# Optimization experiments

Hardware: AMD Instinct MI355X
Metric: run time of the kernel (lower is better)

## Reference

```python
import jax, jax.numpy as jnp
import numpy as np

EPS = 1e-6

def setup_inputs() -> dict:
    key = jax.random.key(0)
    ks = jax.random.split(key, 8)
    I, S, O = 1024, 512, 1024
    Bsz, T = 4, 2048
    return {
        "u": jax.random.normal(ks[0], (Bsz, T, I), dtype=jnp.float32),
        "dt": jax.random.normal(ks[1], (S,), dtype=jnp.float32),
        "A": jax.random.normal(ks[2], (S,), dtype=jnp.float32),
        "Bmat": jax.random.normal(ks[3], (I, S), dtype=jnp.float32) / np.sqrt(S),
        "C": jax.random.normal(ks[4], (S, O), dtype=jnp.float32) / np.sqrt(S),
        "D": jax.random.normal(ks[5], (O,), dtype=jnp.float32),
        "norm_w": jnp.ones((I,), dtype=jnp.float32),
    }

def _rmsnorm(x, w):
    x32 = x.astype(jnp.float32)
    n = x32 * jax.lax.rsqrt(jnp.mean(x32 * x32, axis=-1, keepdims=True) + EPS)
    return n.astype(x.dtype) * w

def reference(u, dt, A, Bmat, C, D, norm_w):
    u = _rmsnorm(u, norm_w)                      # [B, T, I]
    Bsz, T, _ = u.shape
    dts = jax.nn.sigmoid(dt)                     # [S]
    a = jnp.exp(-dts * jnp.abs(A))               # [S] discretized decay
    t = jnp.arange(T, dtype=jnp.float32)
    h = dts[:, None] * a[:, None] ** t[None, :]  # [S, T] geometric kernel
    u_proj = jnp.einsum('bti,is->bst', u, Bmat)  # [B, S, T]
    # depthwise causal conv: flipped kernel + cross-correlation == convolution
    k = jnp.flip(h, axis=1)[:, None, :]          # [S, 1, T] (OIW)
    x = jax.lax.conv_general_dilated(
        u_proj, k, window_strides=(1,), padding=[(T - 1, T - 1)],
        dimension_numbers=('NCW', 'OIW', 'NCW'),
        feature_group_count=u_proj.shape[1])[:, :, :T]  # [B, S, T]
    x = jnp.transpose(x, (0, 2, 1))              # [B, T, S]
    y = jnp.einsum('bts,so->bto', x, C) + D      # [B, T, O]
    return (y, x[:, -1])
```

## Files before the change

kernel.cpp:

```cpp
#include <hip/hip_runtime.h>
#include <math.h>

#define I_DIM 1024
#define S_DIM 512
#define O_DIM 1024
#define T_DIM 2048
#define B_SZ 4
#define M_ROWS (B_SZ * T_DIM)
#define EPSF 1e-6f

#define CL 64
#define NCH 32

typedef _Float16 f16;
typedef __attribute__((ext_vector_type(8))) _Float16 f16x8;
typedef __attribute__((ext_vector_type(2))) _Float16 f16x2;
typedef __attribute__((ext_vector_type(4))) float f32x4;

__device__ __forceinline__ unsigned short f2h_bits(float f) {
    _Float16 h = (_Float16)f;
    return __builtin_bit_cast(unsigned short, h);
}

__device__ __forceinline__ void load16_lds(const void* g, void* l) {
    __builtin_amdgcn_global_load_lds((const __attribute__((address_space(1))) void*)g,
                                     (__attribute__((address_space(3))) void*)l,
                                     16, 0, 0);
}

__global__ __launch_bounds__(256)
void prep(const float* __restrict__ u, const float* __restrict__ nw,
          unsigned short* __restrict__ u16,
          const float* __restrict__ Bmat, const float* __restrict__ dt,
          unsigned short* __restrict__ Bt16,
          const float* __restrict__ Cmat, unsigned short* __restrict__ Ct16) {
    __shared__ float tile[32][33];
    const int t = threadIdx.x;
    const int bx = blockIdx.x;

    if (bx < M_ROWS) {
        float4 v = ((const float4*)(u + (size_t)bx * I_DIM))[t];
        float ss = v.x * v.x + v.y * v.y + v.z * v.z + v.w * v.w;
        #pragma unroll
        for (int off = 32; off > 0; off >>= 1) ss += __shfl_down(ss, off, 64);
        if ((t & 63) == 0) tile[0][t >> 6] = ss;
        __syncthreads();
        if (t == 0)
            tile[0][0] = rsqrtf((tile[0][0] + tile[0][1] + tile[0][2] + tile[0][3])
                                * (1.0f / I_DIM) + EPSF);
        __syncthreads();
        const float rs = tile[0][0];
        float4 w = ((const float4*)nw)[t];
        ushort4 o;
        o.x = f2h_bits(v.x * rs * w.x);
        o.y = f2h_bits(v.y * rs * w.y);
        o.z = f2h_bits(v.z * rs * w.z);
        o.w = f2h_bits(v.w * rs * w.w);
        ((ushort4*)(u16 + (size_t)bx * I_DIM))[t] = o;
    } else if (bx < M_ROWS + 512) {
        const int tb = bx - M_ROWS;
        const int bs = (tb & 15) * 32;
        const int bi = (tb >> 4) * 32;
        const int tx = t & 31, ty = t >> 5;
        #pragma unroll
        for (int i = ty; i < 32; i += 8)
            tile[i][tx] = Bmat[(size_t)(bi + i) * S_DIM + bs + tx];
        __syncthreads();
        #pragma unroll
        for (int i = ty; i < 32; i += 8) {
            const int s = bs + i;
            const float dts = 1.0f / (1.0f + expf(-dt[s]));
            Bt16[(size_t)s * I_DIM + bi + tx] = f2h_bits(tile[tx][i] * dts);
        }
    } else {
        const int tb = bx - M_ROWS - 512;
        const int bo = (tb & 31) * 32;
        const int bs = (tb >> 5) * 32;
        const int tx = t & 31, ty = t >> 5;
        #pragma unroll
        for (int i = ty; i < 32; i += 8)
            tile[i][tx] = Cmat[(size_t)(bs + i) * O_DIM + bo + tx];
        __syncthreads();
        #pragma unroll
        for (int i = ty; i < 32; i += 8)
            Ct16[(size_t)(bo + i) * S_DIM + bs + tx] = f2h_bits(tile[tx][i]);
    }
}

template<bool BIAS, bool CHFIN, typename OUT>
__global__ __launch_bounds__(256)
void mfma_gemm_f16(const f16* __restrict__ A, const f16* __restrict__ Bt,
                   OUT* __restrict__ Cout, int M, int N, int K, int ldb,
                   const float* __restrict__ bias,
                   const float* __restrict__ dt, const float* __restrict__ Avec,
                   float* __restrict__ chlast) {
    constexpr int BM = 64, BN = 128;
    __shared__ f16 As[2][BM * 32];
    __shared__ f16 Bs[2][BN * 32];
    const int t = threadIdx.x;

    int bid = blockIdx.y * gridDim.x + blockIdx.x;
    const int nwg = gridDim.x * gridDim.y;
    const int cpx = nwg >> 3;
    bid = (bid & 7) * cpx + (bid >> 3);
    const int n0 = (bid % gridDim.x) * BN;
    const int m0 = (bid / gridDim.x) * BM;

    const int wid = t >> 6, lane = t & 63;
    const int wn = wid * 32;
    const int lr = lane & 15, kg = lane >> 4;

    f32x4 acc[4][2];
    #pragma unroll
    for (int i = 0; i < 4; ++i)
        #pragma unroll
        for (int j = 0; j < 2; ++j) acc[i][j] = (f32x4){0.f, 0.f, 0.f, 0.f};

    const size_t arow = (size_t)(m0 + (t >> 2)) * K + (t & 3) * 8;
    const size_t brow = (size_t)(n0 + (t >> 2)) * ldb + (t & 3) * 8;

    auto stage = [&](int k0, int bsel) {
        load16_lds(A + arow + k0, &As[bsel][t * 8]);
        load16_lds(Bt + brow + k0, &Bs[bsel][t * 8]);
        load16_lds(Bt + brow + (size_t)64 * ldb + k0, &Bs[bsel][2048 + t * 8]);
    };

    const int nk = K >> 5;
    stage(0, 0);
    for (int kt = 0; kt < nk; ++kt) {
        const int cur = kt & 1;
        if (kt + 1 < nk) {
            stage((kt + 1) << 5, cur ^ 1);
            asm volatile("s_waitcnt vmcnt(3)");
        } else {
            asm volatile("s_waitcnt vmcnt(0)");
        }
        __builtin_amdgcn_s_barrier();
        __builtin_amdgcn_sched_barrier(0);

        f16x8 af[4], bfr[2];
        #pragma unroll
        for (int m = 0; m < 4; ++m)
            af[m] = *(const f16x8*)&As[cur][(m * 16 + lr) * 32 + kg * 8];
        #pragma unroll
        for (int n = 0; n < 2; ++n)
            bfr[n] = *(const f16x8*)&Bs[cur][(wn + n * 16 + lr) * 32 + kg * 8];
        #pragma unroll
        for (int m = 0; m < 4; ++m)
            #pragma unroll
            for (int n = 0; n < 2; ++n)
                acc[m][n] = __builtin_amdgcn_mfma_f32_16x16x32_f16(af[m], bfr[n], acc[m][n], 0, 0, 0);
        __builtin_amdgcn_s_barrier();
    }

    #pragma unroll
    for (int m = 0; m < 4; ++m) {
        const int row = m0 + m * 16 + kg * 4;
        #pragma unroll
        for (int n = 0; n < 2; ++n) {
            const int col = n0 + wn + n * 16 + lr;
            const float b = BIAS ? bias[col] : 0.0f;
            #pragma unroll
            for (int j = 0; j < 4; ++j) {
                if constexpr (sizeof(OUT) == 4)
                    Cout[(size_t)(row + j) * N + col] = (OUT)(acc[m][n][j] + b);
                else
                    Cout[(size_t)(row + j) * N + col] = (OUT)(_Float16)acc[m][n][j];
            }
        }
    }

    if constexpr (CHFIN) {
        const int cb = m0 >> 11;
        const int cc = (m0 >> 6) & (NCH - 1);
        #pragma unroll
        for (int n = 0; n < 2; ++n) {
            const int s = n0 + wn + n * 16 + lr;
            const float dts = 1.0f / (1.0f + expf(-dt[s]));
            const float e = dts * fabsf(Avec[s]);
            const float ainv = expf(e);
            float partial = 0.f;
            #pragma unroll
            for (int m = 0; m < 4; ++m) {
                float wgt = expf(-e * (float)(63 - m * 16 - kg * 4));
                #pragma unroll
                for (int j = 0; j < 4; ++j) {
                    partial = fmaf(wgt, acc[m][n][j], partial);
                    wgt *= ainv;
                }
            }
            partial += __shfl_xor(partial, 16, 64);
            partial += __shfl_xor(partial, 32, 64);
            if (kg == 0)
                chlast[(size_t)(cb * NCH + cc) * S_DIM + s] = partial;
        }
    }
}

__global__ __launch_bounds__(256)
void scan_apply(const f16* __restrict__ up, const float* __restrict__ chlast,
                const float* __restrict__ dt, const float* __restrict__ Avec,
                unsigned* __restrict__ x32, float* __restrict__ xlast) {
    const int gid = blockIdx.x * 256 + threadIdx.x;
    const int s2 = gid & 255;
    const int c = (gid >> 8) & (NCH - 1);
    const int b = gid >> 13;
    const int s0 = s2 * 2;
    const float dts0 = 1.0f / (1.0f + expf(-dt[s0]));
    const float dts1 = 1.0f / (1.0f + expf(-dt[s0 + 1]));
    const float ab0 = fabsf(Avec[s0]), ab1 = fabsf(Avec[s0 + 1]);
    const float a0 = expf(-dts0 * ab0);
    const float a1 = expf(-dts1 * ab1);
    const float aCL0 = expf(-dts0 * ab0 * (float)CL);
    const float aCL1 = expf(-dts1 * ab1 * (float)CL);

    const float2* ch = (const float2*)chlast;
    float cy0 = 0.f, cy1 = 0.f;
    for (int j = 0; j < c; ++j) {
        float2 f = ch[(size_t)(b * NCH + j) * 256 + s2];
        cy0 = fmaf(aCL0, cy0, f.x);
        cy1 = fmaf(aCL1, cy1, f.y);
    }

    const unsigned* up32 = (const unsigned*)up;
    const size_t base = (size_t)(b * T_DIM + c * CL) * 256 + s2;
    unsigned v[CL];
    #pragma unroll
    for (int j = 0; j < CL; ++j) v[j] = up32[base + (size_t)j * 256];
    float x0 = cy0, x1 = cy1;
    #pragma unroll
    for (int j = 0; j < CL; ++j) {
        f16x2 h = __builtin_bit_cast(f16x2, v[j]);
        x0 = fmaf(a0, x0, (float)h.x);
        x1 = fmaf(a1, x1, (float)h.y);
        f16x2 o; o.x = (_Float16)x0; o.y = (_Float16)x1;
        v[j] = __builtin_bit_cast(unsigned, o);
    }
    #pragma unroll
    for (int j = 0; j < CL; ++j) x32[base + (size_t)j * 256] = v[j];
    if (c == NCH - 1) ((float2*)xlast)[b * 256 + s2] = make_float2(x0, x1);
}

extern "C" void kernel_launch(void* const* d_in, const int* in_sizes, int n_in,
                              void* d_out, int out_size, void* d_ws, size_t ws_size,
                              hipStream_t stream) {
    const float* u    = (const float*)d_in[0];
    const float* dt   = (const float*)d_in[1];
    const float* Avec = (const float*)d_in[2];
    const float* Bmat = (const float*)d_in[3];
    const float* Cmat = (const float*)d_in[4];
    const float* Dvec = (const float*)d_in[5];
    const float* nw   = (const float*)d_in[6];

    float* y     = (float*)d_out;
    float* xlast = y + (size_t)M_ROWS * O_DIM;

    char* w = (char*)d_ws;
    unsigned short* u16    = (unsigned short*)(w);
    f16*            up16   = (f16*)(w + 16777216);
    f16*            x16    = (f16*)(w + 25165824);
    unsigned short* Bt16   = (unsigned short*)(w + 33554432);
    unsigned short* Ct16   = (unsigned short*)(w + 34603008);
    float*          chlast = (float*)(w + 35651584);

    prep<<<M_ROWS + 512 + 512, 256, 0, stream>>>(u, nw, u16, Bmat, dt, Bt16, Cmat, Ct16);

    dim3 g1(S_DIM / 128, M_ROWS / 64);
    mfma_gemm_f16<false, true, f16><<<g1, 256, 0, stream>>>(
        (const f16*)u16, (const f16*)Bt16, up16, M_ROWS, S_DIM, I_DIM, I_DIM,
        nullptr, dt, Avec, chlast);

    scan_apply<<<(B_SZ * NCH * 256) / 256, 256, 0, stream>>>(up16, chlast, dt, Avec,
                                                             (unsigned*)x16, xlast);

    dim3 g2(O_DIM / 128, M_ROWS / 64);
    mfma_gemm_f16<true, false, float><<<g2, 256, 0, stream>>>(
        x16, (const f16*)Ct16, y, M_ROWS, O_DIM, S_DIM, S_DIM,
        Dvec, nullptr, nullptr, nullptr);
}
```

Measured before the change: 65.07 us.

## Fuse RMSNorm into GEMM1 and chunk scan into GEMM2 prologue

```diff
diff --git a/kernel.cpp b/kernel.cpp
--- a/kernel.cpp
+++ b/kernel.cpp
@@ -29,54 +29,31 @@
 }
 
 __global__ __launch_bounds__(256)
-void prep(const float* __restrict__ u, const float* __restrict__ nw,
-          unsigned short* __restrict__ u16,
-          const float* __restrict__ Bmat, const float* __restrict__ dt,
-          unsigned short* __restrict__ Bt16,
-          const float* __restrict__ Cmat, unsigned short* __restrict__ Ct16) {
+void prep_w(const float* __restrict__ Bmat, const float* __restrict__ dt,
+            const float* __restrict__ nw, unsigned short* __restrict__ Bt16,
+            const float* __restrict__ Cmat, unsigned short* __restrict__ Ct16) {
     __shared__ float tile[32][33];
     const int t = threadIdx.x;
+    const int tx = t & 31, ty = t >> 5;
     const int bx = blockIdx.x;
-
-    if (bx < M_ROWS) {
-        float4 v = ((const float4*)(u + (size_t)bx * I_DIM))[t];
-        float ss = v.x * v.x + v.y * v.y + v.z * v.z + v.w * v.w;
-        #pragma unroll
-        for (int off = 32; off > 0; off >>= 1) ss += __shfl_down(ss, off, 64);
-        if ((t & 63) == 0) tile[0][t >> 6] = ss;
-        __syncthreads();
-        if (t == 0)
-            tile[0][0] = rsqrtf((tile[0][0] + tile[0][1] + tile[0][2] + tile[0][3])
-                                * (1.0f / I_DIM) + EPSF);
-        __syncthreads();
-        const float rs = tile[0][0];
-        float4 w = ((const float4*)nw)[t];
-        ushort4 o;
-        o.x = f2h_bits(v.x * rs * w.x);
-        o.y = f2h_bits(v.y * rs * w.y);
-        o.z = f2h_bits(v.z * rs * w.z);
-        o.w = f2h_bits(v.w * rs * w.w);
-        ((ushort4*)(u16 + (size_t)bx * I_DIM))[t] = o;
-    } else if (bx < M_ROWS + 512) {
-        const int tb = bx - M_ROWS;
-        const int bs = (tb & 15) * 32;
-        const int bi = (tb >> 4) * 32;
-        const int tx = t & 31, ty = t >> 5;
+    if (bx < 512) {
+        const int bs = (bx & 15) * 32;
+        const int bi = (bx >> 4) * 32;
         #pragma unroll
         for (int i = ty; i < 32; i += 8)
             tile[i][tx] = Bmat[(size_t)(bi + i) * S_DIM + bs + tx];
         __syncthreads();
+        const float w = nw[bi + tx];
         #pragma unroll
         for (int i = ty; i < 32; i += 8) {
             const int s = bs + i;
             const float dts = 1.0f / (1.0f + expf(-dt[s]));
-            Bt16[(size_t)s * I_DIM + bi + tx] = f2h_bits(tile[tx][i] * dts);
+            Bt16[(size_t)s * I_DIM + bi + tx] = f2h_bits(tile[tx][i] * dts * w);
         }
     } else {
-        const int tb = bx - M_ROWS - 512;
+        const int tb = bx - 512;
         const int bo = (tb & 31) * 32;
         const int bs = (tb >> 5) * 32;
-        const int tx = t & 31, ty = t >> 5;
         #pragma unroll
         for (int i = ty; i < 32; i += 8)
             tile[i][tx] = Cmat[(size_t)(bs + i) * O_DIM + bo + tx];
@@ -87,158 +64,211 @@
     }
 }
 
-template<bool BIAS, bool CHFIN, typename OUT>
 __global__ __launch_bounds__(256)
-void mfma_gemm_f16(const f16* __restrict__ A, const f16* __restrict__ Bt,
-                   OUT* __restrict__ Cout, int M, int N, int K, int ldb,
-                   const float* __restrict__ bias,
-                   const float* __restrict__ dt, const float* __restrict__ Avec,
-                   float* __restrict__ chlast) {
-    constexpr int BM = 64, BN = 128;
-    __shared__ f16 As[2][BM * 32];
-    __shared__ f16 Bs[2][BN * 32];
+void gemm1_rms_chfin(const float* __restrict__ U, const f16* __restrict__ Bt,
+                     f16* __restrict__ up, float* __restrict__ chlast,
+                     const float* __restrict__ dt, const float* __restrict__ Avec) {
+    constexpr int K = I_DIM, N = S_DIM, LDA = 80, NK = K / 32;
+    __shared__ __align__(16) unsigned char AsB[2][64 * LDA];
+    __shared__ f16 Bs[2][128 * 32];
+    __shared__ float rsbuf[64];
     const int t = threadIdx.x;
 
-    int bid = blockIdx.y * gridDim.x + blockIdx.x;
-    const int nwg = gridDim.x * gridDim.y;
-    const int cpx = nwg >> 3;
-    bid = (bid & 7) * cpx + (bid >> 3);
-    const int n0 = (bid % gridDim.x) * BN;
-    const int m0 = (bid / gridDim.x) * BM;
-
+    int bid = blockIdx.x;
+    bid = (bid & 7) * 64 + (bid >> 3);
+    const int n0 = (bid & 3) * 128;
+    const int m0 = (bid >> 2) * 64;
     const int wid = t >> 6, lane = t & 63;
-    const int wn = wid * 32;
-    const int lr = lane & 15, kg = lane >> 4;
-
+    const int wn = wid * 32, lr = lane & 15, kg = lane >> 4;
+
+    const float* aptr = U + (size_t)(m0 + (t >> 2)) * K + (t & 3) * 8;
+    const f16*  bptr = Bt + (size_t)(n0 + (t >> 2)) * K + (t & 3) * 8;
+    unsigned char* adst0 = &AsB[0][(t >> 2) * LDA + (t & 3) * 16];
+    unsigned char* adst1 = &AsB[1][(t >> 2) * LDA + (t & 3) * 16];
+
+    float ss = 0.f;
     f32x4 acc[4][2];
     #pragma unroll
     for (int i = 0; i < 4; ++i)
         #pragma unroll
         for (int j = 0; j < 2; ++j) acc[i][j] = (f32x4){0.f, 0.f, 0.f, 0.f};
 
-    const size_t arow = (size_t)(m0 + (t >> 2)) * K + (t & 3) * 8;
-    const size_t brow = (size_t)(n0 + (t >> 2)) * ldb + (t & 3) * 8;
-
-    auto stage = [&](int k0, int bsel) {
-        load16_lds(A + arow + k0, &As[bsel][t * 8]);
-        load16_lds(Bt + brow + k0, &Bs[bsel][t * 8]);
-        load16_lds(Bt + brow + (size_t)64 * ldb + k0, &Bs[bsel][2048 + t * 8]);
+    float4 ra, rb;
+    auto cvt_write = [&](unsigned char* dst) {
+        ss += ra.x * ra.x + ra.y * ra.y + ra.z * ra.z + ra.w * ra.w
+            + rb.x * rb.x + rb.y * rb.y + rb.z * rb.z + rb.w * rb.w;
+        f16x8 h = { (_Float16)ra.x, (_Float16)ra.y, (_Float16)ra.z, (_Float16)ra.w,
+                    (_Float16)rb.x, (_Float16)rb.y, (_Float16)rb.z, (_Float16)rb.w };
+        *(f16x8*)dst = h;
     };
 
-    const int nk = K >> 5;
-    stage(0, 0);
-    for (int kt = 0; kt < nk; ++kt) {
+    load16_lds(bptr, &Bs[0][t * 8]);
+    load16_lds(bptr + (size_t)64 * K, &Bs[0][2048 + t * 8]);
+    ra = *(const float4*)(aptr);
+    rb = *(const float4*)(aptr + 4);
+    cvt_write(adst0);
+    __syncthreads();
+
+    for (int kt = 0; kt < NK; ++kt) {
         const int cur = kt & 1;
-        if (kt + 1 < nk) {
-            stage((kt + 1) << 5, cur ^ 1);
-            asm volatile("s_waitcnt vmcnt(3)");
-        } else {
-            asm volatile("s_waitcnt vmcnt(0)");
-        }
-        __builtin_amdgcn_s_barrier();
-        __builtin_amdgcn_sched_barrier(0);
-
-        f16x8 af[4], bfr[2];
+        if (kt + 1 < NK) {
+            const int k1 = (kt + 1) * 32;
+            load16_lds(bptr + k1, &Bs[cur ^ 1][t * 8]);
+            load16_lds(bptr + (size_t)64 * K + k1, &Bs[cur ^ 1][2048 + t * 8]);
+            ra = *(const float4*)(aptr + k1);
+            rb = *(const float4*)(aptr + k1 + 4);
+        }
+        f16x8 af[4], bf[2];
         #pragma unroll
         for (int m = 0; m < 4; ++m)
-            af[m] = *(const f16x8*)&As[cur][(m * 16 + lr) * 32 + kg * 8];
+            af[m] = *(const f16x8*)&AsB[cur][(m * 16 + lr) * LDA + kg * 16];
         #pragma unroll
         for (int n = 0; n < 2; ++n)
-            bfr[n] = *(const f16x8*)&Bs[cur][(wn + n * 16 + lr) * 32 + kg * 8];
+            bf[n] = *(const f16x8*)&Bs[cur][(wn + n * 16 + lr) * 32 + kg * 8];
         #pragma unroll
         for (int m = 0; m < 4; ++m)
             #pragma unroll
             for (int n = 0; n < 2; ++n)
-                acc[m][n] = __builtin_amdgcn_mfma_f32_16x16x32_f16(af[m], bfr[n], acc[m][n], 0, 0, 0);
-        __builtin_amdgcn_s_barrier();
-    }
-
-    #pragma unroll
-    for (int m = 0; m < 4; ++m) {
-        const int row = m0 + m * 16 + kg * 4;
-        #pragma unroll
-        for (int n = 0; n < 2; ++n) {
-            const int col = n0 + wn + n * 16 + lr;
-            const float b = BIAS ? bias[col] : 0.0f;
+                acc[m][n] = __builtin_amdgcn_mfma_f32_16x16x32_f16(af[m], bf[n], acc[m][n], 0, 0, 0);
+        if (kt + 1 < NK) cvt_write(cur == 0 ? adst1 : adst0);
+        __syncthreads();
+    }
+
+    ss += __shfl_xor(ss, 1, 64);
+    ss += __shfl_xor(ss, 2, 64);
+    if ((t & 3) == 0) rsbuf[t >> 2] = rsqrtf(ss * (1.0f / K) + EPSF);
+    __syncthreads();
+
+    const int cb = m0 >> 11;
+    const int cc = (m0 >> 6) & (NCH - 1);
+    #pragma unroll
+    for (int n = 0; n < 2; ++n) {
+        const int col = n0 + wn + n * 16 + lr;
+        const float dts = 1.0f / (1.0f + expf(-dt[col]));
+        const float e = dts * fabsf(Avec[col]);
+        const float ainv = expf(e);
+        float partial = 0.f;
+        #pragma unroll
+        for (int m = 0; m < 4; ++m) {
+            const int row = m * 16 + kg * 4;
+            f32x4 rs4 = *(const f32x4*)&rsbuf[row];
+            float wgt = expf(-e * (float)(63 - row));
             #pragma unroll
             for (int j = 0; j < 4; ++j) {
-                if constexpr (sizeof(OUT) == 4)
-                    Cout[(size_t)(row + j) * N + col] = (OUT)(acc[m][n][j] + b);
-                else
-                    Cout[(size_t)(row + j) * N + col] = (OUT)(_Float16)acc[m][n][j];
+                const float val = rs4[j] * acc[m][n][j];
+                up[(size_t)(m0 + row + j) * N + col] = (_Float16)val;
+                partial = fmaf(wgt, val, partial);
+                wgt *= ainv;
             }
         }
-    }
-
-    if constexpr (CHFIN) {
-        const int cb = m0 >> 11;
-        const int cc = (m0 >> 6) & (NCH - 1);
-        #pragma unroll
-        for (int n = 0; n < 2; ++n) {
-            const int s = n0 + wn + n * 16 + lr;
-            const float dts = 1.0f / (1.0f + expf(-dt[s]));
-            const float e = dts * fabsf(Avec[s]);
-            const float ainv = expf(e);
-            float partial = 0.f;
-            #pragma unroll
-            for (int m = 0; m < 4; ++m) {
-                float wgt = expf(-e * (float)(63 - m * 16 - kg * 4));
-                #pragma unroll
-                for (int j = 0; j < 4; ++j) {
-                    partial = fmaf(wgt, acc[m][n][j], partial);
-                    wgt *= ainv;
-                }
-            }
-            partial += __shfl_xor(partial, 16, 64);
-            partial += __shfl_xor(partial, 32, 64);
-            if (kg == 0)
-                chlast[(size_t)(cb * NCH + cc) * S_DIM + s] = partial;
-        }
+        partial += __shfl_xor(partial, 16, 64);
+        partial += __shfl_xor(partial, 32, 64);
+        if (kg == 0)
+            chlast[(size_t)(cb * NCH + cc) * S_DIM + col] = partial;
     }
 }
 
 __global__ __launch_bounds__(256)
-void scan_apply(const f16* __restrict__ up, const float* __restrict__ chlast,
+void gemm2_scan(const f16* __restrict__ upb, const float* __restrict__ chlast,
+                const f16* __restrict__ Ct, const float* __restrict__ Dvec,
                 const float* __restrict__ dt, const float* __restrict__ Avec,
-                unsigned* __restrict__ x32, float* __restrict__ xlast) {
-    const int gid = blockIdx.x * 256 + threadIdx.x;
-    const int s2 = gid & 255;
-    const int c = (gid >> 8) & (NCH - 1);
-    const int b = gid >> 13;
-    const int s0 = s2 * 2;
+                float* __restrict__ y, float* __restrict__ xlast) {
+    constexpr int K = S_DIM, N = O_DIM, NK = K / 32;
+    __shared__ __align__(16) unsigned char As[64 * 1024];
+    __shared__ f16 Bs[2][128 * 32];
+    const int t = threadIdx.x;
+
+    int bid = blockIdx.x;
+    bid = (bid & 7) * 128 + (bid >> 3);
+    const int n0 = (bid & 7) * 128;
+    const int m0 = (bid >> 3) * 64;
+    const int wid = t >> 6, lane = t & 63;
+    const int wn = wid * 32, lr = lane & 15, kg = lane >> 4;
+
+    const f16* bptr = Ct + (size_t)(n0 + (t >> 2)) * K + (t & 3) * 8;
+    load16_lds(bptr, &Bs[0][t * 8]);
+    load16_lds(bptr + (size_t)64 * K, &Bs[0][2048 + t * 8]);
+
+    const int cc = (m0 >> 6) & (NCH - 1);
+    const int cb = m0 >> 11;
+    const int s0 = 2 * t;
     const float dts0 = 1.0f / (1.0f + expf(-dt[s0]));
     const float dts1 = 1.0f / (1.0f + expf(-dt[s0 + 1]));
     const float ab0 = fabsf(Avec[s0]), ab1 = fabsf(Avec[s0 + 1]);
-    const float a0 = expf(-dts0 * ab0);
-    const float a1 = expf(-dts1 * ab1);
-    const float aCL0 = expf(-dts0 * ab0 * (float)CL);
-    const float aCL1 = expf(-dts1 * ab1 * (float)CL);
-
+    const float g0 = expf(-dts0 * ab0);
+    const float g1 = expf(-dts1 * ab1);
+    const float gCL0 = expf(-dts0 * ab0 * (float)CL);
+    const float gCL1 = expf(-dts1 * ab1 * (float)CL);
     const float2* ch = (const float2*)chlast;
     float cy0 = 0.f, cy1 = 0.f;
-    for (int j = 0; j < c; ++j) {
-        float2 f = ch[(size_t)(b * NCH + j) * 256 + s2];
-        cy0 = fmaf(aCL0, cy0, f.x);
-        cy1 = fmaf(aCL1, cy1, f.y);
-    }
-
-    const unsigned* up32 = (const unsigned*)up;
-    const size_t base = (size_t)(b * T_DIM + c * CL) * 256 + s2;
+    for (int j = 0; j < cc; ++j) {
+        float2 f = ch[(size_t)(cb * NCH + j) * 256 + t];
+        cy0 = fmaf(gCL0, cy0, f.x);
+        cy1 = fmaf(gCL1, cy1, f.y);
+    }
+
+    const unsigned* up32 = (const unsigned*)upb;
+    const size_t ub = (size_t)m0 * 256 + t;
     unsigned v[CL];
     #pragma unroll
-    for (int j = 0; j < CL; ++j) v[j] = up32[base + (size_t)j * 256];
+    for (int j = 0; j < CL; ++j) v[j] = up32[ub + (size_t)j * 256];
     float x0 = cy0, x1 = cy1;
     #pragma unroll
     for (int j = 0; j < CL; ++j) {
         f16x2 h = __builtin_bit_cast(f16x2, v[j]);
-        x0 = fmaf(a0, x0, (float)h.x);
-        x1 = fmaf(a1, x1, (float)h.y);
+        x0 = fmaf(g0, x0, (float)h.x);
+        x1 = fmaf(g1, x1, (float)h.y);
         f16x2 o; o.x = (_Float16)x0; o.y = (_Float16)x1;
         v[j] = __builtin_bit_cast(unsigned, o);
     }
     #pragma unroll
-    for (int j = 0; j < CL; ++j) x32[base + (size_t)j * 256] = v[j];
-    if (c == NCH - 1) ((float2*)xlast)[b * 256 + s2] = make_float2(x0, x1);
+    for (int j = 0; j < CL; ++j)
+        *(unsigned*)&As[j * 1024 + ((t * 4) ^ ((j & 7) << 4))] = v[j];
+    if (cc == NCH - 1)
+        ((float2*)xlast)[cb * 256 + t] = make_float2(x0, x1);
+    __syncthreads();
+
+    f32x4 acc[4][2];
+    #pragma unroll
+    for (int i = 0; i < 4; ++i)
+        #pragma unroll
+        for (int j = 0; j < 2; ++j) acc[i][j] = (f32x4){0.f, 0.f, 0.f, 0.f};
+
+    const int swz = (lr & 7) << 4;
+    for (int kt = 0; kt < NK; ++kt) {
+        const int cur = kt & 1;
+        if (kt + 1 < NK) {
+            const int k1 = (kt + 1) * 32;
+            load16_lds(bptr + k1, &Bs[cur ^ 1][t * 8]);
+            load16_lds(bptr + (size_t)64 * K + k1, &Bs[cur ^ 1][2048 + t * 8]);
+        }
+        f16x8 af[4], bf[2];
+        #pragma unroll
+        for (int m = 0; m < 4; ++m)
+            af[m] = *(const f16x8*)&As[(m * 16 + lr) * 1024 + ((kt * 64 + kg * 16) ^ swz)];
+        #pragma unroll
+        for (int n = 0; n < 2; ++n)
+            bf[n] = *(const f16x8*)&Bs[cur][(wn + n * 16 + lr) * 32 + kg * 8];
+        #pragma unroll
+        for (int m = 0; m < 4; ++m)
+            #pragma unroll
+            for (int n = 0; n < 2; ++n)
+                acc[m][n] = __builtin_amdgcn_mfma_f32_16x16x32_f16(af[m], bf[n], acc[m][n], 0, 0, 0);
+        __syncthreads();
+    }
+
+    #pragma unroll
+    for (int n = 0; n < 2; ++n) {
+        const int col = n0 + wn + n * 16 + lr;
+        const float dv = Dvec[col];
+        #pragma unroll
+        for (int m = 0; m < 4; ++m) {
+            const int row = m0 + m * 16 + kg * 4;
+            #pragma unroll
+            for (int j = 0; j < 4; ++j)
+                y[(size_t)(row + j) * N + col] = acc[m][n][j] + dv;
+        }
+    }
 }
 
 extern "C" void kernel_launch(void* const* d_in, const int* in_sizes, int n_in,
@@ -256,25 +286,15 @@
     float* xlast = y + (size_t)M_ROWS * O_DIM;
 
     char* w = (char*)d_ws;
-    unsigned short* u16    = (unsigned short*)(w);
-    f16*            up16   = (f16*)(w + 16777216);
-    f16*            x16    = (f16*)(w + 25165824);
-    unsigned short* Bt16   = (unsigned short*)(w + 33554432);
-    unsigned short* Ct16   = (unsigned short*)(w + 34603008);
-    float*          chlast = (float*)(w + 35651584);
-
-    prep<<<M_ROWS + 512 + 512, 256, 0, stream>>>(u, nw, u16, Bmat, dt, Bt16, Cmat, Ct16);
-
-    dim3 g1(S_DIM / 128, M_ROWS / 64);
-    mfma_gemm_f16<false, true, f16><<<g1, 256, 0, stream>>>(
-        (const f16*)u16, (const f16*)Bt16, up16, M_ROWS, S_DIM, I_DIM, I_DIM,
-        nullptr, dt, Avec, chlast);
-
-    scan_apply<<<(B_SZ * NCH * 256) / 256, 256, 0, stream>>>(up16, chlast, dt, Avec,
-                                                             (unsigned*)x16, xlast);
-
-    dim3 g2(O_DIM / 128, M_ROWS / 64);
-    mfma_gemm_f16<true, false, float><<<g2, 256, 0, stream>>>(
-        x16, (const f16*)Ct16, y, M_ROWS, O_DIM, S_DIM, S_DIM,
-        Dvec, nullptr, nullptr, nullptr);
-}
+    f16*            up16   = (f16*)(w);
+    unsigned short* Bt16   = (unsigned short*)(w + 8388608);
+    unsigned short* Ct16   = (unsigned short*)(w + 9437184);
+    float*          chlast = (float*)(w + 10485760);
+
+    prep_w<<<1024, 256, 0, stream>>>(Bmat, dt, nw, Bt16, Cmat, Ct16);
+
+    gemm1_rms_chfin<<<512, 256, 0, stream>>>(u, (const f16*)Bt16, up16, chlast, dt, Avec);
+
+    gemm2_scan<<<1024, 256, 0, stream>>>(up16, chlast, (const f16*)Ct16, Dvec,
+                                         dt, Avec, y, xlast);
+}
```

New measurement: 64.44 us. Within noise of the previous version (-1.0%).
